# Performance work log

Hardware: AMD Instinct MI355X
Metric: run time of the kernel (lower is better)

Reference implementation:

```python
import jax, jax.numpy as jnp
import numpy as np

N = 100000      # nodes
E = 1600000     # directed edges (before self loops)
F_IN = 128      # n_features
H = 100         # hidden width of every GCNConv / fc1
N_HIDDEN = 8    # conv2..conv9


def setup_inputs() -> dict:
    key = jax.random.key(0)
    ks = jax.random.split(key, 12)
    s = 0.05
    x = jax.random.normal(ks[0], (N, F_IN), jnp.float32)
    edge_index = jax.random.randint(ks[1], (2, E), 0, N, dtype=jnp.int64)
    labels = (jax.random.uniform(ks[2], (N, 1)) < 0.1).astype(jnp.float32)
    W1 = jax.random.normal(ks[3], (F_IN, H), jnp.float32) * s
    b1 = jnp.zeros((H,), jnp.float32)
    Wh = jax.random.normal(ks[4], (N_HIDDEN, H, H), jnp.float32) * s
    bh = jnp.zeros((N_HIDDEN, H), jnp.float32)
    fc1_W = jax.random.normal(ks[5], (H, H), jnp.float32) * s
    fc1_b = jnp.zeros((H,), jnp.float32)
    fc2_W = jax.random.normal(ks[6], (H, 1), jnp.float32) * s
    fc2_b = jnp.zeros((1,), jnp.float32)
    return {"x": x, "edge_index": edge_index, "labels": labels,
            "W1": W1, "b1": b1, "Wh": Wh, "bh": bh,
            "fc1_W": fc1_W, "fc1_b": fc1_b, "fc2_W": fc2_W, "fc2_b": fc2_b}


def _gcn_conv(h, W, b, src, dst, norm):
    # linear transform, then degree-normalized scatter aggregation (PyG GCNConv)
    h = h @ W                                   # [N, H]
    msg = h[src] * norm[:, None]                # [E2, H] gather + scale
    agg = jax.ops.segment_sum(msg, dst, num_segments=N)  # scatter-add to [N, H]
    return agg + b


def reference(x, edge_index, labels, W1, b1, Wh, bh, fc1_W, fc1_b, fc2_W, fc2_b):
    # GCN normalization with self loops: norm_e = deg^-1/2[src] * deg^-1/2[dst]
    loops = jnp.arange(N, dtype=edge_index.dtype)
    src = jnp.concatenate([edge_index[0], loops])
    dst = jnp.concatenate([edge_index[1], loops])
    deg = jax.ops.segment_sum(jnp.ones_like(dst, jnp.float32), dst, num_segments=N)
    dinv = jax.lax.rsqrt(deg)                   # deg >= 1 due to self loops
    norm = dinv[src] * dinv[dst]

    # NOTE: source uses x.relu() (out-of-place, discarded) -> no nonlinearity;
    # dropout is identity in eval mode. Faithful reproduction below.
    h = _gcn_conv(x, W1, b1, src, dst, norm)
    for i in range(N_HIDDEN):
        h = _gcn_conv(h, Wh[i], bh[i], src, dst, norm)

    h = h @ fc1_W + fc1_b
    logits = h @ fc2_W + fc2_b
    p = jax.nn.sigmoid(logits)                  # [N, 1]

    # generate_weights: upweight positives by neg/pos ratio
    pos = labels.sum()
    w = ((jnp.float32(N) - pos) / pos) * labels + 1.0

    pc = jnp.clip(p, 1e-7, 1.0 - 1e-7)
    bce = -(labels * jnp.log(pc) + (1.0 - labels) * jnp.log(1.0 - pc))
    loss = jnp.mean(w * bce)
    return loss, p
```

## Files before the change

kernel.cpp:

```cpp
#include <hip/hip_runtime.h>
#include <hip/hip_fp16.h>
#include <math.h>

#define HW 100
#define FIN 128
#define NBLK 256
#define TPB 1024
#define CHUNK 392
#define PBLK 500
#define SLICE 3200
#define SL4 800
#define ELDS 7424
#define M17 0x1FFFFu
#define NPADH 100352

typedef int iv4 __attribute__((ext_vector_type(4)));

__device__ __forceinline__ float ld_dev(const float* p) {
    return __hip_atomic_load(p, __ATOMIC_RELAXED, __HIP_MEMORY_SCOPE_AGENT);
}
__device__ __forceinline__ unsigned ld_devu(const unsigned* p) {
    return __hip_atomic_load(p, __ATOMIC_RELAXED, __HIP_MEMORY_SCOPE_AGENT);
}
__device__ __forceinline__ void st_devu(unsigned* p, unsigned v) {
    __hip_atomic_store(p, v, __ATOMIC_RELAXED, __HIP_MEMORY_SCOPE_AGENT);
}
__device__ __forceinline__ void st_devh(__half* p, __half v) {
    __hip_atomic_store(reinterpret_cast<unsigned short*>(p),
                       *reinterpret_cast<unsigned short*>(&v),
                       __ATOMIC_RELAXED, __HIP_MEMORY_SCOPE_AGENT);
}

__global__ __launch_bounds__(256) void k_prep(const int* __restrict__ src,
                                              const int* __restrict__ dst,
                                              unsigned* __restrict__ buckets,
                                              int* __restrict__ cntG, int* __restrict__ ofsG,
                                              float* __restrict__ accums,
                                              unsigned* __restrict__ posDone,
                                              unsigned* __restrict__ fin,
                                              unsigned* __restrict__ flags,
                                              const float* __restrict__ W1, const float* __restrict__ b1,
                                              const float* __restrict__ Wh, const float* __restrict__ bh,
                                              const float* __restrict__ fc1W, const float* __restrict__ fc1b,
                                              const float* __restrict__ fc2W, const float* __restrict__ fc2b,
                                              float* __restrict__ wstar, float* __restrict__ gammas) {
    int tid = threadIdx.x;
    if (blockIdx.x == 0) {
        __shared__ float v[HW], vn[HW];
        for (int i = tid; i < NBLK * 16; i += 256) flags[i] = 0u;
        if (tid < HW) v[tid] = fc2W[tid];
        __syncthreads();
        if (tid < HW) { float a = 0.f; for (int c = 0; c < HW; ++c) a += fc1W[tid * HW + c] * v[c]; vn[tid] = a; }
        __syncthreads();
        if (tid < HW) v[tid] = vn[tid];
        __syncthreads();
        if (tid == 0) {
            float a = 0.f; for (int c = 0; c < HW; ++c) a += bh[7 * HW + c] * v[c];
            float b = 0.f; for (int c = 0; c < HW; ++c) b += fc1b[c] * fc2W[c];
            gammas[9] = a + b + fc2b[0];
        }
        __syncthreads();
        for (int i = 7; i >= 0; --i) {
            const float* M = Wh + (size_t)i * HW * HW;
            if (tid < HW) { float a = 0.f; for (int c = 0; c < HW; ++c) a += M[tid * HW + c] * v[c]; vn[tid] = a; }
            __syncthreads();
            if (tid < HW) v[tid] = vn[tid];
            __syncthreads();
            if (tid == 0) {
                const float* bb = (i >= 1) ? (bh + (size_t)(i - 1) * HW) : b1;
                float a = 0.f; for (int c = 0; c < HW; ++c) a += bb[c] * v[c];
                gammas[i + 1] = a;
            }
            __syncthreads();
        }
        if (tid < FIN) { float a = 0.f; for (int c = 0; c < HW; ++c) a += W1[tid * HW + c] * v[c]; wstar[tid] = a; }
        if (tid == 0) { accums[0] = 0.f; accums[1] = 0.f; *posDone = 0u; *fin = 0u; }
        return;
    }
    __shared__ int cur[NBLK], wr[NBLK];
    int p = blockIdx.x - 1;
    if (tid < NBLK) cur[tid] = 0;
    __syncthreads();
    const iv4* d4 = reinterpret_cast<const iv4*>(dst) + (size_t)p * SL4;
    const iv4* s4 = reinterpret_cast<const iv4*>(src) + (size_t)p * SL4;
    for (int i = tid; i < SL4; i += 256) {
        iv4 d = d4[i];
        #pragma unroll
        for (int q = 0; q < 4; ++q) {
            unsigned dd = (unsigned)d[q];
            unsigned c = (unsigned)(((unsigned long long)dd * 171634ull) >> 26);
            atomicAdd(&cur[c], 1);
        }
    }
    __syncthreads();
    {
        __shared__ int sc[NBLK];
        if (tid < NBLK) sc[tid] = cur[tid];
        __syncthreads();
        for (int off = 1; off < NBLK; off <<= 1) {
            int v = (tid < NBLK && tid >= off) ? sc[tid - off] : 0;
            __syncthreads();
            if (tid < NBLK) sc[tid] += v;
            __syncthreads();
        }
        if (tid < NBLK) {
            int o = sc[tid] - cur[tid];
            wr[tid] = o;
            cntG[(size_t)p * NBLK + tid] = cur[tid];
            ofsG[(size_t)p * NBLK + tid] = o;
        }
    }
    __syncthreads();
    unsigned* out = buckets + (size_t)p * SLICE;
    for (int i = tid; i < SL4; i += 256) {
        iv4 d = d4[i];
        iv4 s = s4[i];
        #pragma unroll
        for (int q = 0; q < 4; ++q) {
            unsigned dd = (unsigned)d[q];
            unsigned ss = (unsigned)s[q];
            unsigned c = (unsigned)(((unsigned long long)dd * 171634ull) >> 26);
            unsigned ldst = dd - c * 391u;
            int pos = atomicAdd(&wr[c], 1);
            out[pos] = ss | (ldst << 17);
        }
    }
}

__global__ __launch_bounds__(TPB) void k_main(const float* __restrict__ x,
        const float* __restrict__ labels,
        const float* __restrict__ wstar, const float* __restrict__ gammas,
        const int* __restrict__ cntG, const int* __restrict__ ofsG,
        const unsigned* __restrict__ bucketsG,
        __half* __restrict__ ubase,
        float* __restrict__ accums, unsigned* __restrict__ flags,
        unsigned* __restrict__ posDone, unsigned* __restrict__ fin,
        float* __restrict__ outF, int N) {
    __shared__ alignas(16) float ws[FIN];
    __shared__ float gam[16];
    __shared__ int   cntL[512], incl[512], ofsL[512];
    __shared__ int   degLi[CHUNK];
    __shared__ float dinvL[CHUNK], uownL[CHUNK], yownL[CHUNK], accL[CHUNK];
    __shared__ float red[TPB];
    __shared__ alignas(16) unsigned myE[ELDS];

    int tid = threadIdx.x;
    int b = blockIdx.x;
    int chunk = (N + NBLK - 1) / NBLK;
    int nlo = b * chunk; if (nlo > N) nlo = N;
    int nhi = nlo + chunk; if (nhi > N) nhi = N;
    int nn = nhi - nlo;

    if (tid < FIN) ws[tid] = wstar[tid];
    if (tid < 16) gam[tid] = gammas[tid];
    for (int r = tid; r < CHUNK; r += TPB) degLi[r] = 0;
    if (tid < 512) {
        int v = (tid < PBLK) ? cntG[(size_t)tid * NBLK + b] : 0;
        cntL[tid] = v; incl[tid] = v;
        ofsL[tid] = (tid < PBLK) ? ofsG[(size_t)tid * NBLK + b] : 0;
    }
    __syncthreads();
    for (int off = 1; off < 512; off <<= 1) {
        int v = (tid < 512 && tid >= off) ? incl[tid - off] : 0;
        __syncthreads();
        if (tid < 512) incl[tid] += v;
        __syncthreads();
    }
    int ecnt = incl[511];
    if (ecnt > ELDS) ecnt = ELDS;

    for (int p = tid; p < PBLK; p += TPB) {
        int c = cntL[p];
        int g = p * SLICE + ofsL[p];
        int lb = incl[p] - c;
        for (int j = 0; j < c; ++j) {
            unsigned e = bucketsG[g + j];
            if (lb + j < ELDS) { myE[lb + j] = e; atomicAdd(&degLi[e >> 17], 1); }
        }
    }
    __syncthreads();
    for (int r = tid; r < nn; r += TPB) dinvL[r] = rsqrtf((float)degLi[r] + 1.0f);
    __syncthreads();

    {
        int wid = tid >> 6, half = (tid >> 5) & 1, l32 = tid & 31;
        int pcnt = (nn + 1) >> 1;
        const float4* x4 = reinterpret_cast<const float4*>(x);
        for (int pb = wid; pb < pcnt; pb += 16) {
            int ln = pb * 2 + half;
            float dsum = 0.f;
            if (ln < nn) {
                float4 xv = x4[(size_t)(nlo + ln) * (FIN / 4) + l32];
                float4 wv = *reinterpret_cast<const float4*>(&ws[l32 * 4]);
                dsum = xv.x * wv.x + xv.y * wv.y + xv.z * wv.z + xv.w * wv.w;
            }
            #pragma unroll
            for (int off = 16; off; off >>= 1) dsum += __shfl_down(dsum, off, 32);
            if (l32 == 0 && ln < nn) {
                float u0 = dsum * dinvL[ln];
                uownL[ln] = u0;
                st_devh(&ubase[nlo + ln], __float2half(u0));
            }
        }
    }
    asm volatile("s_waitcnt vmcnt(0)" ::: "memory");
    {
        float s = 0.f;
        for (int ln = tid; ln < nn; ln += TPB) s += labels[nlo + ln];
        red[tid] = s; __syncthreads();
        for (int off = TPB / 2; off; off >>= 1) {
            if (tid < off) red[tid] += red[tid + off];
            __syncthreads();
        }
        if (tid == 0) {
            atomicAdd(&accums[0], red[0]);
            asm volatile("s_waitcnt vmcnt(0)" ::: "memory");
            __hip_atomic_fetch_add(posDone, 1u, __ATOMIC_RELAXED, __HIP_MEMORY_SCOPE_AGENT);
            st_devu(&flags[b * 16], 1u);
        }
    }

    for (int k = 1; k <= 9; ++k) {
        const __half* ubr = ubase + (size_t)(k - 1) * NPADH;
        __half* ubw = ubase + (size_t)k * NPADH;
        float gk = gam[k];
        for (int ln = tid; ln < nn; ln += TPB) accL[ln] = uownL[ln];
        if (tid < NBLK)
            while (ld_devu(&flags[tid * 16]) < (unsigned)k) __builtin_amdgcn_s_sleep(1);
        __syncthreads();
        int ecnt8 = ecnt & ~7;
        for (int e = tid * 8; e < ecnt8; e += TPB * 8) {
            uint4 pA = *reinterpret_cast<const uint4*>(&myE[e]);
            uint4 pB = *reinterpret_cast<const uint4*>(&myE[e + 4]);
            float f0 = __half2float(ubr[pA.x & M17]);
            float f1 = __half2float(ubr[pA.y & M17]);
            float f2 = __half2float(ubr[pA.z & M17]);
            float f3 = __half2float(ubr[pA.w & M17]);
            float f4 = __half2float(ubr[pB.x & M17]);
            float f5 = __half2float(ubr[pB.y & M17]);
            float f6 = __half2float(ubr[pB.z & M17]);
            float f7 = __half2float(ubr[pB.w & M17]);
            atomicAdd(&accL[pA.x >> 17], f0);
            atomicAdd(&accL[pA.y >> 17], f1);
            atomicAdd(&accL[pA.z >> 17], f2);
            atomicAdd(&accL[pA.w >> 17], f3);
            atomicAdd(&accL[pB.x >> 17], f4);
            atomicAdd(&accL[pB.y >> 17], f5);
            atomicAdd(&accL[pB.z >> 17], f6);
            atomicAdd(&accL[pB.w >> 17], f7);
        }
        for (int e = ecnt8 + tid; e < ecnt; e += TPB) {
            unsigned p = myE[e];
            atomicAdd(&accL[p >> 17], __half2float(ubr[p & M17]));
        }
        __syncthreads();
        for (int ln = tid; ln < nn; ln += TPB) {
            float di = dinvL[ln];
            float y = di * accL[ln] + gk;
            float nu = di * y;
            uownL[ln] = nu;
            if (k < 9) st_devh(&ubw[nlo + ln], __float2half(nu));
            else yownL[ln] = y;
        }
        if (k < 9) {
            asm volatile("s_waitcnt vmcnt(0)" ::: "memory");
            __syncthreads();
            if (tid == 0) st_devu(&flags[b * 16], (unsigned)(k + 1));
        }
    }
    __syncthreads();

    if (tid == 0)
        while (ld_devu(posDone) < NBLK) __builtin_amdgcn_s_sleep(2);
    __syncthreads();
    {
        float pos = ld_dev(&accums[0]);
        float wpos = ((float)N - pos) / pos;
        float acc = 0.f;
        for (int ln = tid; ln < nn; ln += TPB) {
            float y = yownL[ln];
            float pp = 1.f / (1.f + expf(-y));
            outF[1 + nlo + ln] = pp;
            float pc = fminf(fmaxf(pp, 1e-7f), 1.f - 1e-7f);
            float l = labels[nlo + ln];
            float w = wpos * l + 1.f;
            acc += w * (-(l * logf(pc) + (1.f - l) * logf(1.f - pc)));
        }
        red[tid] = acc; __syncthreads();
        for (int off = TPB / 2; off; off >>= 1) {
            if (tid < off) red[tid] += red[tid + off];
            __syncthreads();
        }
        if (tid == 0) {
            atomicAdd(&accums[1], red[0]);
            asm volatile("s_waitcnt vmcnt(0)" ::: "memory");
            unsigned old = __hip_atomic_fetch_add(fin, 1u, __ATOMIC_RELAXED, __HIP_MEMORY_SCOPE_AGENT);
            if (old == NBLK - 1u)
                outF[0] = ld_dev(&accums[1]) / (float)N;
        }
    }
}

extern "C" void kernel_launch(void* const* d_in, const int* in_sizes, int n_in,
                              void* d_out, int out_size, void* d_ws, size_t ws_size,
                              hipStream_t stream) {
    const float* x      = (const float*)d_in[0];
    const int*   edge   = (const int*)d_in[1];
    const float* labels = (const float*)d_in[2];
    const float* W1     = (const float*)d_in[3];
    const float* b1     = (const float*)d_in[4];
    const float* Wh     = (const float*)d_in[5];
    const float* bh     = (const float*)d_in[6];
    const float* fc1W   = (const float*)d_in[7];
    const float* fc1b   = (const float*)d_in[8];
    const float* fc2W   = (const float*)d_in[9];
    const float* fc2b   = (const float*)d_in[10];

    const int N = in_sizes[0] / FIN;
    const int E = in_sizes[1] / 2;
    const int* srcIdx = edge;
    const int* dstIdx = edge + E;

    size_t o = 0;
    auto carve = [&](size_t bytes) {
        void* p = (char*)d_ws + o;
        o += (bytes + 511) & ~(size_t)511;
        return p;
    };
    float*    accums  = (float*)   carve(4 * 4);
    unsigned* posDone = (unsigned*)carve(4);
    unsigned* fin     = (unsigned*)carve(4);
    unsigned* flags   = (unsigned*)carve((size_t)NBLK * 16 * 4);
    float*    wstar   = (float*)   carve(FIN * 4);
    float*    gammas  = (float*)   carve(16 * 4);
    __half*   ubase   = (__half*)  carve((size_t)NPADH * 10 * 2);
    int*      cnt     = (int*)     carve((size_t)PBLK * NBLK * 4);
    int*      ofs     = (int*)     carve((size_t)PBLK * NBLK * 4);
    unsigned* buckets = (unsigned*)carve((size_t)PBLK * SLICE * 4);
    (void)ws_size; (void)n_in; (void)out_size;

    k_prep<<<PBLK + 1, 256, 0, stream>>>(srcIdx, dstIdx, buckets, cnt, ofs,
                                         accums, posDone, fin, flags,
                                         W1, b1, Wh, bh, fc1W, fc1b, fc2W, fc2b,
                                         wstar, gammas);

    float* outF = (float*)d_out;
    int Nv = N;
    void* args[] = {(void*)&x, (void*)&labels, (void*)&wstar, (void*)&gammas,
                    (void*)&cnt, (void*)&ofs, (void*)&buckets, (void*)&ubase,
                    (void*)&accums, (void*)&flags, (void*)&posDone, (void*)&fin,
                    (void*)&outF, (void*)&Nv};
    hipError_t err = hipLaunchCooperativeKernel((const void*)k_main, dim3(NBLK), dim3(TPB),
                                                args, 0, stream);
    (void)err;
}
```

Baseline: 186.0 us.

## Stage half-precision node vector into LDS in two halves before gather

Each of the nine propagation steps now copies the shared half-precision vector into LDS in two halves and gathers from LDS rather than from random global loads. Edges are pre-partitioned in LDS by source half so each half's edges run after that half is staged. Blocks wait only on the producers of the current half, which may let the first half overlap with slower blocks. This adds about 100KB of extra LDS per block and two bulk copies per layer, and changes the sleep intervals in the spin-waits.

```diff
diff --git a/kernel.cpp b/kernel.cpp
--- a/kernel.cpp
+++ b/kernel.cpp
@@ -13,6 +13,9 @@
 #define ELDS 7424
 #define M17 0x1FFFFu
 #define NPADH 100352
+#define HSPLIT 50048
+#define HV40 6256
+#define HV41 6244
 
 typedef int iv4 __attribute__((ext_vector_type(4)));
 
@@ -143,6 +146,8 @@
     __shared__ float dinvL[CHUNK], uownL[CHUNK], yownL[CHUNK], accL[CHUNK];
     __shared__ float red[TPB];
     __shared__ alignas(16) unsigned myE[ELDS];
+    __shared__ alignas(16) __half uL[HSPLIT];
+    __shared__ int h0c, c0, c1;
 
     int tid = threadIdx.x;
     int b = blockIdx.x;
@@ -159,6 +164,7 @@
         cntL[tid] = v; incl[tid] = v;
         ofsL[tid] = (tid < PBLK) ? ofsG[(size_t)tid * NBLK + b] : 0;
     }
+    if (tid == 0) { h0c = 0; }
     __syncthreads();
     for (int off = 1; off < 512; off <<= 1) {
         int v = (tid < 512 && tid >= off) ? incl[tid - off] : 0;
@@ -179,8 +185,25 @@
         }
     }
     __syncthreads();
+    {
+        unsigned* scr = reinterpret_cast<unsigned*>(uL);
+        for (int e = tid; e < ecnt; e += TPB) {
+            unsigned v = myE[e];
+            scr[e] = v;
+            if ((v & M17) < HSPLIT) atomicAdd(&h0c, 1);
+        }
+        __syncthreads();
+        if (tid == 0) { c0 = 0; c1 = h0c; }
+        __syncthreads();
+        for (int e = tid; e < ecnt; e += TPB) {
+            unsigned v = scr[e];
+            int pos = ((v & M17) < HSPLIT) ? atomicAdd(&c0, 1) : atomicAdd(&c1, 1);
+            myE[pos] = v;
+        }
+    }
     for (int r = tid; r < nn; r += TPB) dinvL[r] = rsqrtf((float)degLi[r] + 1.0f);
     __syncthreads();
+    int seg0 = h0c;
 
     {
         int wid = tid >> 6, half = (tid >> 5) & 1, l32 = tid & 31;
@@ -225,33 +248,31 @@
         __half* ubw = ubase + (size_t)k * NPADH;
         float gk = gam[k];
         for (int ln = tid; ln < nn; ln += TPB) accL[ln] = uownL[ln];
-        if (tid < NBLK)
-            while (ld_devu(&flags[tid * 16]) < (unsigned)k) __builtin_amdgcn_s_sleep(1);
-        __syncthreads();
-        int ecnt8 = ecnt & ~7;
-        for (int e = tid * 8; e < ecnt8; e += TPB * 8) {
-            uint4 pA = *reinterpret_cast<const uint4*>(&myE[e]);
-            uint4 pB = *reinterpret_cast<const uint4*>(&myE[e + 4]);
-            float f0 = __half2float(ubr[pA.x & M17]);
-            float f1 = __half2float(ubr[pA.y & M17]);
-            float f2 = __half2float(ubr[pA.z & M17]);
-            float f3 = __half2float(ubr[pA.w & M17]);
-            float f4 = __half2float(ubr[pB.x & M17]);
-            float f5 = __half2float(ubr[pB.y & M17]);
-            float f6 = __half2float(ubr[pB.z & M17]);
-            float f7 = __half2float(ubr[pB.w & M17]);
-            atomicAdd(&accL[pA.x >> 17], f0);
-            atomicAdd(&accL[pA.y >> 17], f1);
-            atomicAdd(&accL[pA.z >> 17], f2);
-            atomicAdd(&accL[pA.w >> 17], f3);
-            atomicAdd(&accL[pB.x >> 17], f4);
-            atomicAdd(&accL[pB.y >> 17], f5);
-            atomicAdd(&accL[pB.z >> 17], f6);
-            atomicAdd(&accL[pB.w >> 17], f7);
-        }
-        for (int e = ecnt8 + tid; e < ecnt; e += TPB) {
+        if (tid < 128)
+            while (ld_devu(&flags[tid * 16]) < (unsigned)k) __builtin_amdgcn_s_sleep(16);
+        __syncthreads();
+        {
+            const uint4* sv = reinterpret_cast<const uint4*>(ubr);
+            uint4* dv = reinterpret_cast<uint4*>(uL);
+            for (int i = tid; i < HV40; i += TPB) dv[i] = sv[i];
+        }
+        __syncthreads();
+        for (int e = tid; e < seg0; e += TPB) {
             unsigned p = myE[e];
-            atomicAdd(&accL[p >> 17], __half2float(ubr[p & M17]));
+            atomicAdd(&accL[p >> 17], __half2float(uL[p & M17]));
+        }
+        if (tid < 128)
+            while (ld_devu(&flags[(128 + tid) * 16]) < (unsigned)k) __builtin_amdgcn_s_sleep(16);
+        __syncthreads();
+        {
+            const uint4* sv = reinterpret_cast<const uint4*>(ubr + HSPLIT);
+            uint4* dv = reinterpret_cast<uint4*>(uL);
+            for (int i = tid; i < HV41; i += TPB) dv[i] = sv[i];
+        }
+        __syncthreads();
+        for (int e = seg0 + tid; e < ecnt; e += TPB) {
+            unsigned p = myE[e];
+            atomicAdd(&accL[p >> 17], __half2float(uL[(p & M17) - HSPLIT]));
         }
         __syncthreads();
         for (int ln = tid; ln < nn; ln += TPB) {
@@ -271,7 +292,7 @@
     __syncthreads();
 
     if (tid == 0)
-        while (ld_devu(posDone) < NBLK) __builtin_amdgcn_s_sleep(2);
+        while (ld_devu(posDone) < NBLK) __builtin_amdgcn_s_sleep(16);
     __syncthreads();
     {
         float pos = ld_dev(&accums[0]);
```

After: 218.1 us. +17.3%, slower.

## Fuse edge bucketing and weight-chain precompute into the cooperative main kernel

Applied to the files above, without the earlier changes.

Removes the separate k_prep launch and folds its work into the persistent cooperative kernel. Blocks 0-249 each bucket two edge slices, block 255 computes the collapsed weight chain (wstar, gammas), and everyone waits on per-block flags and a chain flag before continuing. The sync counters are zeroed with a memset, and the flag epoch values are shifted by one. This saves a kernel launch and the inter-kernel gap, but bucketing now runs on only 250 blocks inside the main kernel and adds spin-wait dependencies.

```diff
diff --git a/kernel.cpp b/kernel.cpp
--- a/kernel.cpp
+++ b/kernel.cpp
@@ -19,6 +19,9 @@
 __device__ __forceinline__ float ld_dev(const float* p) {
     return __hip_atomic_load(p, __ATOMIC_RELAXED, __HIP_MEMORY_SCOPE_AGENT);
 }
+__device__ __forceinline__ void st_dev(float* p, float v) {
+    __hip_atomic_store(p, v, __ATOMIC_RELAXED, __HIP_MEMORY_SCOPE_AGENT);
+}
 __device__ __forceinline__ unsigned ld_devu(const unsigned* p) {
     return __hip_atomic_load(p, __ATOMIC_RELAXED, __HIP_MEMORY_SCOPE_AGENT);
 }
@@ -31,109 +34,18 @@
                        __ATOMIC_RELAXED, __HIP_MEMORY_SCOPE_AGENT);
 }
 
-__global__ __launch_bounds__(256) void k_prep(const int* __restrict__ src,
-                                              const int* __restrict__ dst,
-                                              unsigned* __restrict__ buckets,
-                                              int* __restrict__ cntG, int* __restrict__ ofsG,
-                                              float* __restrict__ accums,
-                                              unsigned* __restrict__ posDone,
-                                              unsigned* __restrict__ fin,
-                                              unsigned* __restrict__ flags,
-                                              const float* __restrict__ W1, const float* __restrict__ b1,
-                                              const float* __restrict__ Wh, const float* __restrict__ bh,
-                                              const float* __restrict__ fc1W, const float* __restrict__ fc1b,
-                                              const float* __restrict__ fc2W, const float* __restrict__ fc2b,
-                                              float* __restrict__ wstar, float* __restrict__ gammas) {
-    int tid = threadIdx.x;
-    if (blockIdx.x == 0) {
-        __shared__ float v[HW], vn[HW];
-        for (int i = tid; i < NBLK * 16; i += 256) flags[i] = 0u;
-        if (tid < HW) v[tid] = fc2W[tid];
-        __syncthreads();
-        if (tid < HW) { float a = 0.f; for (int c = 0; c < HW; ++c) a += fc1W[tid * HW + c] * v[c]; vn[tid] = a; }
-        __syncthreads();
-        if (tid < HW) v[tid] = vn[tid];
-        __syncthreads();
-        if (tid == 0) {
-            float a = 0.f; for (int c = 0; c < HW; ++c) a += bh[7 * HW + c] * v[c];
-            float b = 0.f; for (int c = 0; c < HW; ++c) b += fc1b[c] * fc2W[c];
-            gammas[9] = a + b + fc2b[0];
-        }
-        __syncthreads();
-        for (int i = 7; i >= 0; --i) {
-            const float* M = Wh + (size_t)i * HW * HW;
-            if (tid < HW) { float a = 0.f; for (int c = 0; c < HW; ++c) a += M[tid * HW + c] * v[c]; vn[tid] = a; }
-            __syncthreads();
-            if (tid < HW) v[tid] = vn[tid];
-            __syncthreads();
-            if (tid == 0) {
-                const float* bb = (i >= 1) ? (bh + (size_t)(i - 1) * HW) : b1;
-                float a = 0.f; for (int c = 0; c < HW; ++c) a += bb[c] * v[c];
-                gammas[i + 1] = a;
-            }
-            __syncthreads();
-        }
-        if (tid < FIN) { float a = 0.f; for (int c = 0; c < HW; ++c) a += W1[tid * HW + c] * v[c]; wstar[tid] = a; }
-        if (tid == 0) { accums[0] = 0.f; accums[1] = 0.f; *posDone = 0u; *fin = 0u; }
-        return;
-    }
-    __shared__ int cur[NBLK], wr[NBLK];
-    int p = blockIdx.x - 1;
-    if (tid < NBLK) cur[tid] = 0;
-    __syncthreads();
-    const iv4* d4 = reinterpret_cast<const iv4*>(dst) + (size_t)p * SL4;
-    const iv4* s4 = reinterpret_cast<const iv4*>(src) + (size_t)p * SL4;
-    for (int i = tid; i < SL4; i += 256) {
-        iv4 d = d4[i];
-        #pragma unroll
-        for (int q = 0; q < 4; ++q) {
-            unsigned dd = (unsigned)d[q];
-            unsigned c = (unsigned)(((unsigned long long)dd * 171634ull) >> 26);
-            atomicAdd(&cur[c], 1);
-        }
-    }
-    __syncthreads();
-    {
-        __shared__ int sc[NBLK];
-        if (tid < NBLK) sc[tid] = cur[tid];
-        __syncthreads();
-        for (int off = 1; off < NBLK; off <<= 1) {
-            int v = (tid < NBLK && tid >= off) ? sc[tid - off] : 0;
-            __syncthreads();
-            if (tid < NBLK) sc[tid] += v;
-            __syncthreads();
-        }
-        if (tid < NBLK) {
-            int o = sc[tid] - cur[tid];
-            wr[tid] = o;
-            cntG[(size_t)p * NBLK + tid] = cur[tid];
-            ofsG[(size_t)p * NBLK + tid] = o;
-        }
-    }
-    __syncthreads();
-    unsigned* out = buckets + (size_t)p * SLICE;
-    for (int i = tid; i < SL4; i += 256) {
-        iv4 d = d4[i];
-        iv4 s = s4[i];
-        #pragma unroll
-        for (int q = 0; q < 4; ++q) {
-            unsigned dd = (unsigned)d[q];
-            unsigned ss = (unsigned)s[q];
-            unsigned c = (unsigned)(((unsigned long long)dd * 171634ull) >> 26);
-            unsigned ldst = dd - c * 391u;
-            int pos = atomicAdd(&wr[c], 1);
-            out[pos] = ss | (ldst << 17);
-        }
-    }
-}
-
-__global__ __launch_bounds__(TPB) void k_main(const float* __restrict__ x,
+__global__ __launch_bounds__(TPB) void k_all(const float* __restrict__ x,
+        const int* __restrict__ src, const int* __restrict__ dst,
         const float* __restrict__ labels,
-        const float* __restrict__ wstar, const float* __restrict__ gammas,
-        const int* __restrict__ cntG, const int* __restrict__ ofsG,
-        const unsigned* __restrict__ bucketsG,
+        const float* __restrict__ W1, const float* __restrict__ b1,
+        const float* __restrict__ Wh, const float* __restrict__ bh,
+        const float* __restrict__ fc1W, const float* __restrict__ fc1b,
+        const float* __restrict__ fc2W, const float* __restrict__ fc2b,
+        unsigned* __restrict__ buckets, int* __restrict__ cntG, int* __restrict__ ofsG,
+        float* __restrict__ wstar, float* __restrict__ gammas,
         __half* __restrict__ ubase,
         float* __restrict__ accums, unsigned* __restrict__ flags,
+        unsigned* __restrict__ chainflag,
         unsigned* __restrict__ posDone, unsigned* __restrict__ fin,
         float* __restrict__ outF, int N) {
     __shared__ alignas(16) float ws[FIN];
@@ -151,8 +63,95 @@
     int nhi = nlo + chunk; if (nhi > N) nhi = N;
     int nn = nhi - nlo;
 
-    if (tid < FIN) ws[tid] = wstar[tid];
-    if (tid < 16) gam[tid] = gammas[tid];
+    if (b < 250) {
+        int* cur = cntL; int* sc = incl; int* wr = ofsL;
+        for (int sl = 0; sl < 2; ++sl) {
+            int p = b * 2 + sl;
+            if (tid < NBLK) cur[tid] = 0;
+            __syncthreads();
+            const iv4* d4 = reinterpret_cast<const iv4*>(dst) + (size_t)p * SL4;
+            const iv4* s4 = reinterpret_cast<const iv4*>(src) + (size_t)p * SL4;
+            iv4 d = {0, 0, 0, 0}, s = {0, 0, 0, 0};
+            if (tid < SL4) {
+                d = __builtin_nontemporal_load(d4 + tid);
+                s = __builtin_nontemporal_load(s4 + tid);
+                #pragma unroll
+                for (int q = 0; q < 4; ++q) {
+                    unsigned dd = (unsigned)d[q];
+                    unsigned c = (unsigned)(((unsigned long long)dd * 171634ull) >> 26);
+                    atomicAdd(&cur[c], 1);
+                }
+            }
+            __syncthreads();
+            if (tid < NBLK) sc[tid] = cur[tid];
+            __syncthreads();
+            for (int off = 1; off < NBLK; off <<= 1) {
+                int v = (tid < NBLK && tid >= off) ? sc[tid - off] : 0;
+                __syncthreads();
+                if (tid < NBLK) sc[tid] += v;
+                __syncthreads();
+            }
+            if (tid < NBLK) {
+                int o = sc[tid] - cur[tid];
+                wr[tid] = o;
+                st_devu((unsigned*)&cntG[(size_t)p * NBLK + tid], (unsigned)cur[tid]);
+                st_devu((unsigned*)&ofsG[(size_t)p * NBLK + tid], (unsigned)o);
+            }
+            __syncthreads();
+            if (tid < SL4) {
+                unsigned* out = buckets + (size_t)p * SLICE;
+                #pragma unroll
+                for (int q = 0; q < 4; ++q) {
+                    unsigned dd = (unsigned)d[q];
+                    unsigned ss = (unsigned)s[q];
+                    unsigned c = (unsigned)(((unsigned long long)dd * 171634ull) >> 26);
+                    unsigned ldst = dd - c * 391u;
+                    int pos = atomicAdd(&wr[c], 1);
+                    st_devu(&out[pos], ss | (ldst << 17));
+                }
+            }
+            __syncthreads();
+        }
+        asm volatile("s_waitcnt vmcnt(0)" ::: "memory");
+        __syncthreads();
+        if (tid == 0) st_devu(&flags[b * 16], 1u);
+    } else if (b == 255) {
+        __shared__ float v[HW], vn[HW];
+        if (tid < HW) v[tid] = fc2W[tid];
+        __syncthreads();
+        if (tid < HW) { float a = 0.f; for (int c = 0; c < HW; ++c) a += fc1W[tid * HW + c] * v[c]; vn[tid] = a; }
+        __syncthreads();
+        if (tid < HW) v[tid] = vn[tid];
+        __syncthreads();
+        if (tid == 0) {
+            float a = 0.f; for (int c = 0; c < HW; ++c) a += bh[7 * HW + c] * v[c];
+            float bb2 = 0.f; for (int c = 0; c < HW; ++c) bb2 += fc1b[c] * fc2W[c];
+            st_dev(&gammas[9], a + bb2 + fc2b[0]);
+        }
+        __syncthreads();
+        for (int i = 7; i >= 0; --i) {
+            const float* M = Wh + (size_t)i * HW * HW;
+            if (tid < HW) { float a = 0.f; for (int c = 0; c < HW; ++c) a += M[tid * HW + c] * v[c]; vn[tid] = a; }
+            __syncthreads();
+            if (tid < HW) v[tid] = vn[tid];
+            __syncthreads();
+            if (tid == 0) {
+                const float* bb = (i >= 1) ? (bh + (size_t)(i - 1) * HW) : b1;
+                float a = 0.f; for (int c = 0; c < HW; ++c) a += bb[c] * v[c];
+                st_dev(&gammas[i + 1], a);
+            }
+            __syncthreads();
+        }
+        if (tid < FIN) { float a = 0.f; for (int c = 0; c < HW; ++c) a += W1[tid * HW + c] * v[c]; st_dev(&wstar[tid], a); }
+        asm volatile("s_waitcnt vmcnt(0)" ::: "memory");
+        __syncthreads();
+        if (tid == 0) st_devu(chainflag, 1u);
+    }
+    __syncthreads();
+
+    if (tid < 250)
+        while (ld_devu(&flags[tid * 16]) < 1u) __builtin_amdgcn_s_sleep(1);
+    __syncthreads();
     for (int r = tid; r < CHUNK; r += TPB) degLi[r] = 0;
     if (tid < 512) {
         int v = (tid < PBLK) ? cntG[(size_t)tid * NBLK + b] : 0;
@@ -168,18 +167,22 @@
     }
     int ecnt = incl[511];
     if (ecnt > ELDS) ecnt = ELDS;
-
     for (int p = tid; p < PBLK; p += TPB) {
         int c = cntL[p];
         int g = p * SLICE + ofsL[p];
         int lb = incl[p] - c;
         for (int j = 0; j < c; ++j) {
-            unsigned e = bucketsG[g + j];
+            unsigned e = buckets[g + j];
             if (lb + j < ELDS) { myE[lb + j] = e; atomicAdd(&degLi[e >> 17], 1); }
         }
     }
     __syncthreads();
     for (int r = tid; r < nn; r += TPB) dinvL[r] = rsqrtf((float)degLi[r] + 1.0f);
+    if (tid == 0)
+        while (ld_devu(chainflag) < 1u) __builtin_amdgcn_s_sleep(1);
+    __syncthreads();
+    if (tid < FIN) ws[tid] = wstar[tid];
+    if (tid < 16) gam[tid] = gammas[tid];
     __syncthreads();
 
     {
@@ -216,7 +219,7 @@
             atomicAdd(&accums[0], red[0]);
             asm volatile("s_waitcnt vmcnt(0)" ::: "memory");
             __hip_atomic_fetch_add(posDone, 1u, __ATOMIC_RELAXED, __HIP_MEMORY_SCOPE_AGENT);
-            st_devu(&flags[b * 16], 1u);
+            st_devu(&flags[b * 16], 2u);
         }
     }
 
@@ -226,7 +229,7 @@
         float gk = gam[k];
         for (int ln = tid; ln < nn; ln += TPB) accL[ln] = uownL[ln];
         if (tid < NBLK)
-            while (ld_devu(&flags[tid * 16]) < (unsigned)k) __builtin_amdgcn_s_sleep(1);
+            while (ld_devu(&flags[tid * 16]) < (unsigned)(k + 1)) __builtin_amdgcn_s_sleep(1);
         __syncthreads();
         int ecnt8 = ecnt & ~7;
         for (int e = tid * 8; e < ecnt8; e += TPB * 8) {
@@ -265,7 +268,7 @@
         if (k < 9) {
             asm volatile("s_waitcnt vmcnt(0)" ::: "memory");
             __syncthreads();
-            if (tid == 0) st_devu(&flags[b * 16], (unsigned)(k + 1));
+            if (tid == 0) st_devu(&flags[b * 16], (unsigned)(k + 2));
         }
     }
     __syncthreads();
@@ -327,30 +330,32 @@
         o += (bytes + 511) & ~(size_t)511;
         return p;
     };
-    float*    accums  = (float*)   carve(4 * 4);
-    unsigned* posDone = (unsigned*)carve(4);
-    unsigned* fin     = (unsigned*)carve(4);
-    unsigned* flags   = (unsigned*)carve((size_t)NBLK * 16 * 4);
+    float*    accums    = (float*)   carve(4 * 4);
+    unsigned* posDone   = (unsigned*)carve(4);
+    unsigned* fin       = (unsigned*)carve(4);
+    unsigned* chainflag = (unsigned*)carve(4);
+    unsigned* flags     = (unsigned*)carve((size_t)NBLK * 16 * 4);
+    size_t syncBytes = o;
     float*    wstar   = (float*)   carve(FIN * 4);
     float*    gammas  = (float*)   carve(16 * 4);
     __half*   ubase   = (__half*)  carve((size_t)NPADH * 10 * 2);
     int*      cnt     = (int*)     carve((size_t)PBLK * NBLK * 4);
     int*      ofs     = (int*)     carve((size_t)PBLK * NBLK * 4);
     unsigned* buckets = (unsigned*)carve((size_t)PBLK * SLICE * 4);
-    (void)ws_size; (void)n_in; (void)out_size;
-
-    k_prep<<<PBLK + 1, 256, 0, stream>>>(srcIdx, dstIdx, buckets, cnt, ofs,
-                                         accums, posDone, fin, flags,
-                                         W1, b1, Wh, bh, fc1W, fc1b, fc2W, fc2b,
-                                         wstar, gammas);
+    (void)ws_size; (void)n_in; (void)out_size; (void)E;
+
+    hipMemsetAsync(d_ws, 0, syncBytes, stream);
 
     float* outF = (float*)d_out;
     int Nv = N;
-    void* args[] = {(void*)&x, (void*)&labels, (void*)&wstar, (void*)&gammas,
-                    (void*)&cnt, (void*)&ofs, (void*)&buckets, (void*)&ubase,
-                    (void*)&accums, (void*)&flags, (void*)&posDone, (void*)&fin,
-                    (void*)&outF, (void*)&Nv};
-    hipError_t err = hipLaunchCooperativeKernel((const void*)k_main, dim3(NBLK), dim3(TPB),
+    void* args[] = {(void*)&x, (void*)&srcIdx, (void*)&dstIdx, (void*)&labels,
+                    (void*)&W1, (void*)&b1, (void*)&Wh, (void*)&bh,
+                    (void*)&fc1W, (void*)&fc1b, (void*)&fc2W, (void*)&fc2b,
+                    (void*)&buckets, (void*)&cnt, (void*)&ofs,
+                    (void*)&wstar, (void*)&gammas, (void*)&ubase,
+                    (void*)&accums, (void*)&flags, (void*)&chainflag,
+                    (void*)&posDone, (void*)&fin, (void*)&outF, (void*)&Nv};
+    hipError_t err = hipLaunchCooperativeKernel((const void*)k_all, dim3(NBLK), dim3(TPB),
                                                 args, 0, stream);
     (void)err;
 }
```

Result: slower. 191.1 us (+2.8%).
